# Optimization experiments

Measured on AMD Instinct MI355X. Metric: run time of the kernel, lower is better.

Reference implementation:

```python
import jax, jax.numpy as jnp
import numpy as np

B, LC, LQ, D = 32, 2048, 256, 256


def setup_inputs() -> dict:
    key = jax.random.key(0)
    kc, kq, kcm, kqm, kw = jax.random.split(key, 5)
    context = jax.random.normal(kc, (B, LC, D), dtype=jnp.float32)
    query = jax.random.normal(kq, (B, LQ, D), dtype=jnp.float32)
    # True = masked (matches torch masked_fill semantics)
    context_mask = jax.random.randint(kcm, (B, LC), 0, 2).astype(bool)
    query_mask = jax.random.randint(kqm, (B, LQ), 0, 2).astype(bool)
    # nn.Linear(3*dim, 1, bias=False) weight, flattened to (3D,)
    w0 = jax.random.normal(kw, (3 * D,), dtype=jnp.float32) * (1.0 / np.sqrt(3 * D))
    return {"context": context, "query": query, "context_mask": context_mask,
            "query_mask": query_mask, "w0": w0}


def reference(context, query, context_mask, query_mask, w0):
    d = context.shape[-1]
    wc, wq, wm = w0[:d], w0[d:2 * d], w0[2 * d:]
    # trilinear sim: w0 . [c, q, c*q]  ==  c.wc + q.wq + (c*wm) q^T
    sc = context @ wc                                   # (B, Lc)
    sq = query @ wq                                     # (B, Lq)
    sim = sc[:, :, None] + sq[:, None, :] + jnp.einsum(
        'bcd,bqd->bcq', context * wm, query)            # (B, Lc, Lq)
    mask = context_mask[:, :, None] | query_mask[:, None, :]
    sim = jnp.where(mask, jnp.float32(-1e30), sim)
    S = jax.nn.softmax(sim, axis=-1)                    # row softmax over Lq
    SS = jax.nn.softmax(sim, axis=1)                    # col softmax over Lc
    S = jnp.nan_to_num(S)
    SS = jnp.nan_to_num(SS)
    A = jnp.einsum('bcq,bqd->bcd', S, query)            # (B, Lc, D)
    T = jnp.einsum('bkq,bkd->bqd', SS, context)         # SS^T @ context, (B, Lq, D)
    Bmat = jnp.einsum('bcq,bqd->bcd', S, T)             # (B, Lc, D)
    return (A, Bmat)
```

## Files before the change

kernel.cpp:

```cpp
#include <hip/hip_runtime.h>

#define B_  32
#define LC_ 2048
#define LQ_ 256
#define D_  256
#define NEGH (-30000.0f)
#define MASKF (-100000.0f)

typedef _Float16 f16;
typedef _Float16 f16x4 __attribute__((ext_vector_type(4)));
typedef _Float16 f16x8 __attribute__((ext_vector_type(8)));
typedef float    f32x4 __attribute__((ext_vector_type(4)));

__global__ __launch_bounds__(256) void k_prepq(
    const float* __restrict__ qry, const float* __restrict__ w0,
    const int* __restrict__ qmask,
    f16* __restrict__ qrywm16, float* __restrict__ sqm,
    f16* __restrict__ Bcat)
{
    __shared__ float tile[32 * 260];
    __shared__ float wm_s[256], wq_s[256];
    const int b = blockIdx.y, q0 = blockIdx.x * 32;
    const int t = threadIdx.x;
    wm_s[t] = w0[2 * D_ + t];
    wq_s[t] = w0[D_ + t];
    __syncthreads();
    const int r = t >> 3, s = t & 7;
    const float* qb = qry + ((long long)(b * LQ_ + q0 + r)) * D_ + s * 32;
    f16* ob = qrywm16 + ((long long)(b * LQ_ + q0 + r)) * D_ + s * 32;
    float dot = 0.f;
    #pragma unroll
    for (int p = 0; p < 8; ++p) {
        float4 v = *(const float4*)(qb + p * 4);
        int cb = s * 32 + p * 4;
        f16x4 h;
        h[0] = (f16)(v.x * wm_s[cb + 0]); h[1] = (f16)(v.y * wm_s[cb + 1]);
        h[2] = (f16)(v.z * wm_s[cb + 2]); h[3] = (f16)(v.w * wm_s[cb + 3]);
        *(f16x4*)(ob + p * 4) = h;
        tile[r * 260 + cb + 0] = v.x;
        tile[r * 260 + cb + 1] = v.y;
        tile[r * 260 + cb + 2] = v.z;
        tile[r * 260 + cb + 3] = v.w;
        dot += v.x * wq_s[cb + 0] + v.y * wq_s[cb + 1]
             + v.z * wq_s[cb + 2] + v.w * wq_s[cb + 3];
    }
    dot += __shfl_xor(dot, 1, 64);
    dot += __shfl_xor(dot, 2, 64);
    dot += __shfl_xor(dot, 4, 64);
    if (s == 0) {
        int q = b * LQ_ + q0 + r;
        sqm[q] = qmask[q] ? MASKF : dot;
    }
    __syncthreads();
    {
        f16* orow = Bcat + (long long)b * 512 * LQ_ + (long long)t * LQ_ + q0;
        #pragma unroll
        for (int qq = 0; qq < 32; qq += 4) {
            f16x4 h;
            h[0] = (f16)tile[(qq + 0) * 260 + t];
            h[1] = (f16)tile[(qq + 1) * 260 + t];
            h[2] = (f16)tile[(qq + 2) * 260 + t];
            h[3] = (f16)tile[(qq + 3) * 260 + t];
            *(f16x4*)(orow + qq) = h;
        }
    }
}

#define LDA1 40
__global__ __launch_bounds__(512) void k_g1(
    const float* __restrict__ ctx, const f16* __restrict__ qrywm16,
    const float* __restrict__ w0, const int* __restrict__ cmask,
    const float* __restrict__ sqm,
    f16* __restrict__ ctxT16, f16* __restrict__ p16, f16* __restrict__ pT16,
    float* __restrict__ rowm, float* __restrict__ rowinvl,
    float* __restrict__ pm, float* __restrict__ pl)
{
    __shared__ f16 As[128 * LDA1];
    __shared__ f16 Bs[256 * LDA1];
    __shared__ float wc_s[256];
    __shared__ float scm_s[128];
    __shared__ float rowpm[4][128], rowps[4][128];
    __shared__ float colpm[2][256], colps[2][256];
    __shared__ float rowmax_s[128], colmax_s[256];
    const int b = blockIdx.z;
    const int c0 = blockIdx.x * 128;
    const int t = threadIdx.x, lane = t & 63, wv = t >> 6;
    const int wm_off = (wv >> 2) * 64, wn_off = (wv & 3) * 64;
    const float* Ab = ctx + ((long long)b * LC_ + c0) * D_;
    const f16* Bb = qrywm16 + (long long)b * LQ_ * D_;
    const int srow = t >> 2, scg = (t & 3) * 8;
    const int td = t & 31, tcc = t >> 5;
    if (t < 256) wc_s[t] = w0[t];
    __syncthreads();
    f32x4 acc[4][4] = {};
    float scdot = 0.f;
    for (int k0 = 0; k0 < D_; k0 += 32) {
        float4 a0 = *(const float4*)(Ab + (long long)srow * D_ + k0 + scg);
        float4 a1 = *(const float4*)(Ab + (long long)srow * D_ + k0 + scg + 4);
        f16x8 ha;
        ha[0] = (f16)a0.x; ha[1] = (f16)a0.y; ha[2] = (f16)a0.z; ha[3] = (f16)a0.w;
        ha[4] = (f16)a1.x; ha[5] = (f16)a1.y; ha[6] = (f16)a1.z; ha[7] = (f16)a1.w;
        scdot += a0.x * wc_s[k0 + scg + 0] + a0.y * wc_s[k0 + scg + 1]
               + a0.z * wc_s[k0 + scg + 2] + a0.w * wc_s[k0 + scg + 3]
               + a1.x * wc_s[k0 + scg + 4] + a1.y * wc_s[k0 + scg + 5]
               + a1.z * wc_s[k0 + scg + 6] + a1.w * wc_s[k0 + scg + 7];
        *(f16x8*)(As + srow * LDA1 + scg) = ha;
        *(f16x8*)(Bs + srow * LDA1 + scg) = *(const f16x8*)(Bb + (long long)srow * D_ + k0 + scg);
        *(f16x8*)(Bs + (srow + 128) * LDA1 + scg) = *(const f16x8*)(Bb + (long long)(srow + 128) * D_ + k0 + scg);
        __syncthreads();
        f16x8 af[4], bf[4];
        #pragma unroll
        for (int i = 0; i < 4; ++i)
            af[i] = *(const f16x8*)(As + (wm_off + i * 16 + (lane & 15)) * LDA1 + (lane >> 4) * 8);
        #pragma unroll
        for (int j = 0; j < 4; ++j)
            bf[j] = *(const f16x8*)(Bs + (wn_off + j * 16 + (lane & 15)) * LDA1 + (lane >> 4) * 8);
        #pragma unroll
        for (int i = 0; i < 4; ++i)
            #pragma unroll
            for (int j = 0; j < 4; ++j)
                acc[i][j] = __builtin_amdgcn_mfma_f32_16x16x32_f16(af[i], bf[j], acc[i][j], 0, 0, 0);
        {
            f16x8 hT;
            #pragma unroll
            for (int j = 0; j < 8; ++j)
                hT[j] = As[(tcc * 8 + j) * LDA1 + td];
            *(f16x8*)(ctxT16 + ((long long)b * D_ + k0 + td) * LC_ + c0 + tcc * 8) = hT;
        }
        __syncthreads();
    }
    scdot += __shfl_xor(scdot, 1, 64);
    scdot += __shfl_xor(scdot, 2, 64);
    if ((t & 3) == 0)
        scm_s[srow] = cmask[b * LC_ + c0 + srow] ? MASKF : scdot;
    __syncthreads();
    float sqv[4];
    #pragma unroll
    for (int j = 0; j < 4; ++j)
        sqv[j] = sqm[b * LQ_ + wn_off + j * 16 + (lane & 15)];
    float scv[4][4];
    #pragma unroll
    for (int i = 0; i < 4; ++i)
        #pragma unroll
        for (int r = 0; r < 4; ++r)
            scv[i][r] = scm_s[wm_off + i * 16 + (lane >> 4) * 4 + r];
    float rmax[4][4], cmax[4];
    #pragma unroll
    for (int i = 0; i < 4; ++i)
        #pragma unroll
        for (int r = 0; r < 4; ++r) rmax[i][r] = -INFINITY;
    #pragma unroll
    for (int j = 0; j < 4; ++j) cmax[j] = -INFINITY;
    #pragma unroll
    for (int i = 0; i < 4; ++i) {
        #pragma unroll
        for (int r = 0; r < 4; ++r) {
            #pragma unroll
            for (int j = 0; j < 4; ++j) {
                float val = fmaxf(acc[i][j][r] + scv[i][r] + sqv[j], NEGH);
                float vr = (float)(f16)val;
                rmax[i][r] = fmaxf(rmax[i][r], vr);
                cmax[j]    = fmaxf(cmax[j], vr);
            }
        }
    }
    #pragma unroll
    for (int i = 0; i < 4; ++i)
        #pragma unroll
        for (int r = 0; r < 4; ++r) {
            rmax[i][r] = fmaxf(rmax[i][r], __shfl_xor(rmax[i][r], 1, 64));
            rmax[i][r] = fmaxf(rmax[i][r], __shfl_xor(rmax[i][r], 2, 64));
            rmax[i][r] = fmaxf(rmax[i][r], __shfl_xor(rmax[i][r], 4, 64));
            rmax[i][r] = fmaxf(rmax[i][r], __shfl_xor(rmax[i][r], 8, 64));
        }
    #pragma unroll
    for (int j = 0; j < 4; ++j) {
        cmax[j] = fmaxf(cmax[j], __shfl_xor(cmax[j], 16, 64));
        cmax[j] = fmaxf(cmax[j], __shfl_xor(cmax[j], 32, 64));
    }
    if ((lane & 15) == 0) {
        #pragma unroll
        for (int i = 0; i < 4; ++i)
            #pragma unroll
            for (int r = 0; r < 4; ++r)
                rowpm[wv & 3][wm_off + i * 16 + (lane >> 4) * 4 + r] = rmax[i][r];
    }
    if (lane < 16) {
        #pragma unroll
        for (int j = 0; j < 4; ++j) colpm[wv >> 2][wn_off + j * 16 + lane] = cmax[j];
    }
    __syncthreads();
    if (t < 128)
        rowmax_s[t] = fmaxf(fmaxf(rowpm[0][t], rowpm[1][t]), fmaxf(rowpm[2][t], rowpm[3][t]));
    if (t < 256)
        colmax_s[t] = fmaxf(colpm[0][t], colpm[1][t]);
    __syncthreads();
    float rmf[4][4], cmf[4];
    #pragma unroll
    for (int i = 0; i < 4; ++i)
        #pragma unroll
        for (int r = 0; r < 4; ++r)
            rmf[i][r] = rowmax_s[wm_off + i * 16 + (lane >> 4) * 4 + r];
    #pragma unroll
    for (int j = 0; j < 4; ++j) cmf[j] = colmax_s[wn_off + j * 16 + (lane & 15)];
    float rsum[4][4] = {}, csum[4] = {};
    #pragma unroll
    for (int i = 0; i < 4; ++i) {
        #pragma unroll
        for (int r = 0; r < 4; ++r) {
            int c = c0 + wm_off + i * 16 + (lane >> 4) * 4 + r;
            f16* prow = p16 + ((long long)b * LC_ + c) * LQ_ + wn_off + (lane & 15);
            #pragma unroll
            for (int j = 0; j < 4; ++j) {
                int q = wn_off + j * 16 + (lane & 15);
                float val = fmaxf(acc[i][j][r] + scv[i][r] + sqv[j], NEGH);
                float vr = (float)(f16)val;
                float er = __expf(vr - rmf[i][r]);
                f16 hp = (f16)er;
                prow[j * 16] = hp;
                pT16[((long long)b * LQ_ + q) * LC_ + c] = hp;
                rsum[i][r] += er;
                csum[j]    += __expf(vr - cmf[j]);
            }
        }
    }
    #pragma unroll
    for (int i = 0; i < 4; ++i)
        #pragma unroll
        for (int r = 0; r < 4; ++r) {
            rsum[i][r] += __shfl_xor(rsum[i][r], 1, 64);
            rsum[i][r] += __shfl_xor(rsum[i][r], 2, 64);
            rsum[i][r] += __shfl_xor(rsum[i][r], 4, 64);
            rsum[i][r] += __shfl_xor(rsum[i][r], 8, 64);
        }
    #pragma unroll
    for (int j = 0; j < 4; ++j) {
        csum[j] += __shfl_xor(csum[j], 16, 64);
        csum[j] += __shfl_xor(csum[j], 32, 64);
    }
    if ((lane & 15) == 0) {
        #pragma unroll
        for (int i = 0; i < 4; ++i)
            #pragma unroll
            for (int r = 0; r < 4; ++r)
                rowps[wv & 3][wm_off + i * 16 + (lane >> 4) * 4 + r] = rsum[i][r];
    }
    if (lane < 16) {
        #pragma unroll
        for (int j = 0; j < 4; ++j) colps[wv >> 2][wn_off + j * 16 + lane] = csum[j];
    }
    __syncthreads();
    if (t < 128) {
        float l = rowps[0][t] + rowps[1][t] + rowps[2][t] + rowps[3][t];
        rowm[b * LC_ + c0 + t]    = rowmax_s[t];
        rowinvl[b * LC_ + c0 + t] = 1.0f / l;
    }
    if (t < 256) {
        int idx = (b * 16 + blockIdx.x) * LQ_ + t;
        pm[idx] = colmax_s[t];
        pl[idx] = colps[0][t] + colps[1][t];
    }
}

__global__ __launch_bounds__(256) void k_colreduce(
    const float* __restrict__ pm, const float* __restrict__ pl,
    float* __restrict__ colm, float* __restrict__ colinvl)
{
    const int col = blockIdx.x * 256 + threadIdx.x;
    const int b = col >> 8, q = col & 255;
    float M = -INFINITY, L = 0.f;
    for (int ch = 0; ch < 16; ++ch) {
        int idx = (b * 16 + ch) * LQ_ + q;
        float m = pm[idx], l = pl[idx];
        float nM = fmaxf(M, m);
        L = L * __expf(M - nM) + l * __expf(m - nM);
        M = nM;
    }
    colm[col] = M; colinvl[col] = 1.0f / L;
}

#define LDA3 72
#define G3SPLIT 4
#define G3CHUNK (LC_ / G3SPLIT)
__global__ __launch_bounds__(512) void k_g3(
    const f16* __restrict__ ctxT16, const f16* __restrict__ pT16,
    const float* __restrict__ rowm, const float* __restrict__ colm,
    float* __restrict__ Tpart)
{
    __shared__ f16 As[128 * LDA3];
    __shared__ f16 Bs[128 * LDA3];
    __shared__ float rowm_s[G3CHUNK];
    __shared__ float colm_s[128];
    const int lin = blockIdx.x;
    const int swz = (lin & 7) * 64 + (lin >> 3);
    const int combo = swz & 3;
    const int split = (swz >> 2) & 3;
    const int b = swz >> 4;
    const int qt = combo & 1, dh = combo >> 1;
    const int q0 = qt * 128, d0 = dh * 128;
    const int cbeg = split * G3CHUNK;
    const int t = threadIdx.x, lane = t & 63, wv = t >> 6;
    const int wm_off = (wv >> 2) * 64, wn_off = (wv & 3) * 32;
    if (t < G3CHUNK) rowm_s[t] = rowm[b * LC_ + cbeg + t];
    if (t < 128) colm_s[t] = colm[b * LQ_ + q0 + t];
    __syncthreads();
    const f16* Ab = ctxT16 + ((long long)b * D_ + d0) * LC_;
    const f16* Pb = pT16 + ((long long)b * LQ_ + q0) * LC_;
    const int ar = t >> 3, acg = (t & 7) * 8;
    f32x4 acc[4][2] = {};
    f16x8 ha[2], hb[2];
    #pragma unroll
    for (int p = 0; p < 2; ++p) {
        ha[p] = *(const f16x8*)(Ab + (long long)(ar + p * 64) * LC_ + cbeg + acg);
        hb[p] = *(const f16x8*)(Pb + (long long)(ar + p * 64) * LC_ + cbeg + acg);
    }
    for (int c0 = cbeg; c0 < cbeg + G3CHUNK; c0 += 64) {
        #pragma unroll
        for (int p = 0; p < 2; ++p) {
            *(f16x8*)(As + (ar + p * 64) * LDA3 + acg) = ha[p];
            float cmq = colm_s[ar + p * 64];
            f16x8 e;
            if (cmq < -29000.f) {
                #pragma unroll
                for (int j = 0; j < 8; ++j) e[j] = (f16)1.0f;
            } else {
                #pragma unroll
                for (int j = 0; j < 8; ++j)
                    e[j] = (f16)((float)hb[p][j] * __expf(rowm_s[(c0 - cbeg) + acg + j] - cmq));
            }
            *(f16x8*)(Bs + (ar + p * 64) * LDA3 + acg) = e;
        }
        if (c0 + 64 < cbeg + G3CHUNK) {
            #pragma unroll
            for (int p = 0; p < 2; ++p) {
                ha[p] = *(const f16x8*)(Ab + (long long)(ar + p * 64) * LC_ + c0 + 64 + acg);
                hb[p] = *(const f16x8*)(Pb + (long long)(ar + p * 64) * LC_ + c0 + 64 + acg);
            }
        }
        __syncthreads();
        #pragma unroll
        for (int kk = 0; kk < 64; kk += 32) {
            f16x8 af[4], bf[2];
            #pragma unroll
            for (int i = 0; i < 4; ++i)
                af[i] = *(const f16x8*)(As + (wm_off + i * 16 + (lane & 15)) * LDA3 + kk + (lane >> 4) * 8);
            #pragma unroll
            for (int j = 0; j < 2; ++j)
                bf[j] = *(const f16x8*)(Bs + (wn_off + j * 16 + (lane & 15)) * LDA3 + kk + (lane >> 4) * 8);
            #pragma unroll
            for (int i = 0; i < 4; ++i)
                #pragma unroll
                for (int j = 0; j < 2; ++j)
                    acc[i][j] = __builtin_amdgcn_mfma_f32_16x16x32_f16(af[i], bf[j], acc[i][j], 0, 0, 0);
        }
        __syncthreads();
    }
    float* Tb = Tpart + ((long long)split * B_ + b) * (LQ_ * D_);
    #pragma unroll
    for (int i = 0; i < 4; ++i) {
        #pragma unroll
        for (int r = 0; r < 4; ++r) {
            int d = d0 + wm_off + i * 16 + (lane >> 4) * 4 + r;
            float* orow = Tb + (long long)d * LQ_ + q0 + wn_off + (lane & 15);
            #pragma unroll
            for (int j = 0; j < 2; ++j)
                orow[j * 16] = acc[i][j][r];
        }
    }
}

__global__ __launch_bounds__(256) void k_bnorm(
    const float* __restrict__ Tpart, const float* __restrict__ colinvl,
    f16* __restrict__ Bcat)
{
    const long long i4 = ((long long)blockIdx.x * 256 + threadIdx.x) * 4;
    const int q = (int)(i4 & 255);
    const int d = (int)((i4 >> 8) & 255);
    const int b = (int)(i4 >> 16);
    float4 s = *(const float4*)(Tpart + i4);
    #pragma unroll
    for (int p = 1; p < G3SPLIT; ++p) {
        float4 v = *(const float4*)(Tpart + (long long)p * (B_ * LQ_ * D_) + i4);
        s.x += v.x; s.y += v.y; s.z += v.z; s.w += v.w;
    }
    float4 ci = *(const float4*)(colinvl + b * LQ_ + q);
    f16x4 h;
    h[0] = (f16)(s.x * ci.x); h[1] = (f16)(s.y * ci.y);
    h[2] = (f16)(s.z * ci.z); h[3] = (f16)(s.w * ci.w);
    *(f16x4*)(Bcat + (long long)b * 512 * LQ_ + (long long)(256 + d) * LQ_ + q) = h;
}

#define LDA23 40
__global__ __launch_bounds__(512) void k_g23(
    const f16* __restrict__ p16, const float* __restrict__ rowinvl,
    const f16* __restrict__ Bcat,
    float* __restrict__ outA, float* __restrict__ outB)
{
    __shared__ f16 As[256 * LDA23];
    __shared__ f16 Bs[256 * LDA23];
    const int lin = blockIdx.x;
    const int swz = (lin & 7) * 64 + (lin >> 3);
    const int cx = swz & 7;
    const int ny = (swz >> 3) & 1;
    const int b  = swz >> 4;
    const int c0 = cx * 256, n0 = ny * 256;
    const int t = threadIdx.x, lane = t & 63, wv = t >> 6;
    const int wm_off = (wv >> 2) * 128;
    const int wn_off = (wv & 3) * 64;
    const f16* Ab = p16 + ((long long)b * LC_ + c0) * LQ_;
    const f16* Bb = Bcat + ((long long)b * 512 + n0) * LQ_;
    const int srow = t >> 2, scg = (t & 3) * 8;
    f32x4 acc[8][4] = {};
    f16x8 ha[2], hb[2];
    #pragma unroll
    for (int p = 0; p < 2; ++p) {
        int r = srow + p * 128;
        ha[p] = *(const f16x8*)(Ab + (long long)r * LQ_ + scg);
        hb[p] = *(const f16x8*)(Bb + (long long)r * LQ_ + scg);
    }
    for (int k0 = 0; k0 < LQ_; k0 += 32) {
        #pragma unroll
        for (int p = 0; p < 2; ++p) {
            int r = srow + p * 128;
            *(f16x8*)(As + r * LDA23 + scg) = ha[p];
            *(f16x8*)(Bs + r * LDA23 + scg) = hb[p];
        }
        if (k0 + 32 < LQ_) {
            #pragma unroll
            for (int p = 0; p < 2; ++p) {
                int r = srow + p * 128;
                ha[p] = *(const f16x8*)(Ab + (long long)r * LQ_ + k0 + 32 + scg);
                hb[p] = *(const f16x8*)(Bb + (long long)r * LQ_ + k0 + 32 + scg);
            }
        }
        __syncthreads();
        f16x8 bf[4];
        #pragma unroll
        for (int j = 0; j < 4; ++j)
            bf[j] = *(const f16x8*)(Bs + (wn_off + j * 16 + (lane & 15)) * LDA23 + (lane >> 4) * 8);
        #pragma unroll
        for (int i = 0; i < 8; ++i) {
            f16x8 af = *(const f16x8*)(As + (wm_off + i * 16 + (lane & 15)) * LDA23 + (lane >> 4) * 8);
            #pragma unroll
            for (int j = 0; j < 4; ++j)
                acc[i][j] = __builtin_amdgcn_mfma_f32_16x16x32_f16(af, bf[j], acc[i][j], 0, 0, 0);
        }
        __syncthreads();
    }
    float* outp = (n0 == 0) ? outA : outB;
    #pragma unroll
    for (int i = 0; i < 8; ++i) {
        #pragma unroll
        for (int r = 0; r < 4; ++r) {
            int c = c0 + wm_off + i * 16 + (lane >> 4) * 4 + r;
            float ri = rowinvl[b * LC_ + c];
            float* orow = outp + ((long long)b * LC_ + c) * D_ + wn_off + (lane & 15);
            #pragma unroll
            for (int j = 0; j < 4; ++j)
                orow[j * 16] = acc[i][j][r] * ri;
        }
    }
}

extern "C" void kernel_launch(void* const* d_in, const int* in_sizes, int n_in,
                              void* d_out, int out_size, void* d_ws, size_t ws_size,
                              hipStream_t stream) {
    const float* ctx   = (const float*)d_in[0];
    const float* qry   = (const float*)d_in[1];
    const int*   cmask = (const int*)d_in[2];
    const int*   qmask = (const int*)d_in[3];
    const float* w0    = (const float*)d_in[4];
    float* out = (float*)d_out;

    char* w = (char*)d_ws;
    float* sqm     = (float*)w;  w += (long long)8192 * 4;
    float* rowm    = (float*)w;  w += (long long)65536 * 4;
    float* rowinvl = (float*)w;  w += (long long)65536 * 4;
    float* colm    = (float*)w;  w += (long long)8192 * 4;
    float* colinvl = (float*)w;  w += (long long)8192 * 4;
    float* pm      = (float*)w;  w += (long long)524288 * 4;
    float* pl      = (float*)w;  w += (long long)524288 * 4;
    f16*   p16     = (f16*)w;    w += (long long)16777216 * 2;
    f16*   pT16    = (f16*)w;    w += (long long)16777216 * 2;
    f16*   ctxT16  = (f16*)w;    w += (long long)16777216 * 2;
    f16*   qrywm16 = (f16*)w;    w += (long long)2097152 * 2;
    f16*   Bcat    = (f16*)w;    w += (long long)4194304 * 2;
    float* Tpart   = (float*)w;  w += (long long)G3SPLIT * 2097152 * 4;

    k_prepq<<<dim3(8, 32), 256, 0, stream>>>(qry, w0, qmask, qrywm16, sqm, Bcat);
    k_g1<<<dim3(16, 1, 32), 512, 0, stream>>>(ctx, qrywm16, w0, cmask, sqm,
        ctxT16, p16, pT16, rowm, rowinvl, pm, pl);
    k_colreduce<<<32, 256, 0, stream>>>(pm, pl, colm, colinvl);
    k_g3<<<512, 512, 0, stream>>>(ctxT16, pT16, rowm, colm, Tpart);
    k_bnorm<<<2048, 256, 0, stream>>>(Tpart, colinvl, Bcat);
    k_g23<<<512, 512, 0, stream>>>(p16, rowinvl, Bcat,
        out, out + (long long)B_ * LC_ * D_);
}
```

Measured before the change: 300.1 us.

## Drop transposed P copy, read row-major P in g3, atomically reduce T splits

k_g1 no longer writes the transposed fp16 probability matrix pT16, which was a scattered 2-byte-stride store of 32 MB. k_g3 now reads row-major p16 and transposes it into shared memory while applying the column-softmax rescale. The four split-K partial T buffers are replaced by one buffer that is zeroed first and accumulated with float atomics, so k_bnorm reads a quarter of the data. Column reduction is also restructured into a two-pass max-then-sum. The costs are scalar 2-byte transposed LDS stores with likely bank conflicts, atomic contention, and a nondeterministic summation order.

Measured after the change: 305.9 us. About the same (+2.0%).

```diff
diff --git a/kernel.cpp b/kernel.cpp
--- a/kernel.cpp
+++ b/kernel.cpp
@@ -11,6 +11,13 @@
 typedef _Float16 f16x4 __attribute__((ext_vector_type(4)));
 typedef _Float16 f16x8 __attribute__((ext_vector_type(8)));
 typedef float    f32x4 __attribute__((ext_vector_type(4)));
+
+__global__ __launch_bounds__(256) void k_zero(float* __restrict__ T)
+{
+    const long long i4 = ((long long)blockIdx.x * 256 + threadIdx.x) * 4;
+    float4 z = {0.f, 0.f, 0.f, 0.f};
+    *(float4*)(T + i4) = z;
+}
 
 __global__ __launch_bounds__(256) void k_prepq(
     const float* __restrict__ qry, const float* __restrict__ w0,
@@ -71,7 +78,7 @@
     const float* __restrict__ ctx, const f16* __restrict__ qrywm16,
     const float* __restrict__ w0, const int* __restrict__ cmask,
     const float* __restrict__ sqm,
-    f16* __restrict__ ctxT16, f16* __restrict__ p16, f16* __restrict__ pT16,
+    f16* __restrict__ ctxT16, f16* __restrict__ p16,
     float* __restrict__ rowm, float* __restrict__ rowinvl,
     float* __restrict__ pm, float* __restrict__ pl)
 {
@@ -212,13 +219,10 @@
             f16* prow = p16 + ((long long)b * LC_ + c) * LQ_ + wn_off + (lane & 15);
             #pragma unroll
             for (int j = 0; j < 4; ++j) {
-                int q = wn_off + j * 16 + (lane & 15);
                 float val = fmaxf(acc[i][j][r] + scv[i][r] + sqv[j], NEGH);
                 float vr = (float)(f16)val;
                 float er = __expf(vr - rmf[i][r]);
-                f16 hp = (f16)er;
-                prow[j * 16] = hp;
-                pT16[((long long)b * LQ_ + q) * LC_ + c] = hp;
+                prow[j * 16] = (f16)er;
                 rsum[i][r] += er;
                 csum[j]    += __expf(vr - cmf[j]);
             }
@@ -268,14 +272,19 @@
 {
     const int col = blockIdx.x * 256 + threadIdx.x;
     const int b = col >> 8, q = col & 255;
-    float M = -INFINITY, L = 0.f;
+    float m[16], l[16];
+    #pragma unroll
     for (int ch = 0; ch < 16; ++ch) {
         int idx = (b * 16 + ch) * LQ_ + q;
-        float m = pm[idx], l = pl[idx];
-        float nM = fmaxf(M, m);
-        L = L * __expf(M - nM) + l * __expf(m - nM);
-        M = nM;
-    }
+        m[ch] = pm[idx];
+        l[ch] = pl[idx];
+    }
+    float M = m[0];
+    #pragma unroll
+    for (int ch = 1; ch < 16; ++ch) M = fmaxf(M, m[ch]);
+    float L = 0.f;
+    #pragma unroll
+    for (int ch = 0; ch < 16; ++ch) L += l[ch] * __expf(m[ch] - M);
     colm[col] = M; colinvl[col] = 1.0f / L;
 }
 
@@ -283,9 +292,9 @@
 #define G3SPLIT 4
 #define G3CHUNK (LC_ / G3SPLIT)
 __global__ __launch_bounds__(512) void k_g3(
-    const f16* __restrict__ ctxT16, const f16* __restrict__ pT16,
+    const f16* __restrict__ ctxT16, const f16* __restrict__ p16,
     const float* __restrict__ rowm, const float* __restrict__ colm,
-    float* __restrict__ Tpart)
+    float* __restrict__ T)
 {
     __shared__ f16 As[128 * LDA3];
     __shared__ f16 Bs[128 * LDA3];
@@ -305,37 +314,37 @@
     if (t < 128) colm_s[t] = colm[b * LQ_ + q0 + t];
     __syncthreads();
     const f16* Ab = ctxT16 + ((long long)b * D_ + d0) * LC_;
-    const f16* Pb = pT16 + ((long long)b * LQ_ + q0) * LC_;
+    const f16* Pb = p16 + (long long)b * LC_ * LQ_;
     const int ar = t >> 3, acg = (t & 7) * 8;
+    const int cr = lane, qg = wv;
     f32x4 acc[4][2] = {};
-    f16x8 ha[2], hb[2];
-    #pragma unroll
-    for (int p = 0; p < 2; ++p) {
-        ha[p] = *(const f16x8*)(Ab + (long long)(ar + p * 64) * LC_ + cbeg + acg);
-        hb[p] = *(const f16x8*)(Pb + (long long)(ar + p * 64) * LC_ + cbeg + acg);
-    }
+    f16x8 ha[2], hbq[2];
+    ha[0] = *(const f16x8*)(Ab + (long long)(ar +  0) * LC_ + cbeg + acg);
+    ha[1] = *(const f16x8*)(Ab + (long long)(ar + 64) * LC_ + cbeg + acg);
+    hbq[0] = *(const f16x8*)(Pb + (long long)(cbeg + cr) * LQ_ + q0 + qg * 16);
+    hbq[1] = *(const f16x8*)(Pb + (long long)(cbeg + cr) * LQ_ + q0 + qg * 16 + 8);
     for (int c0 = cbeg; c0 < cbeg + G3CHUNK; c0 += 64) {
-        #pragma unroll
-        for (int p = 0; p < 2; ++p) {
-            *(f16x8*)(As + (ar + p * 64) * LDA3 + acg) = ha[p];
-            float cmq = colm_s[ar + p * 64];
-            f16x8 e;
-            if (cmq < -29000.f) {
+        *(f16x8*)(As + (ar +  0) * LDA3 + acg) = ha[0];
+        *(f16x8*)(As + (ar + 64) * LDA3 + acg) = ha[1];
+        {
+            float rmv = rowm_s[(c0 - cbeg) + cr];
+            #pragma unroll
+            for (int u = 0; u < 2; ++u) {
                 #pragma unroll
-                for (int j = 0; j < 8; ++j) e[j] = (f16)1.0f;
-            } else {
-                #pragma unroll
-                for (int j = 0; j < 8; ++j)
-                    e[j] = (f16)((float)hb[p][j] * __expf(rowm_s[(c0 - cbeg) + acg + j] - cmq));
+                for (int k = 0; k < 8; ++k) {
+                    int qq = qg * 16 + u * 8 + k;
+                    float cmq = colm_s[qq];
+                    float v = (cmq < -29000.f) ? 1.0f
+                            : (float)hbq[u][k] * __expf(rmv - cmq);
+                    Bs[qq * LDA3 + cr] = (f16)v;
+                }
             }
-            *(f16x8*)(Bs + (ar + p * 64) * LDA3 + acg) = e;
         }
         if (c0 + 64 < cbeg + G3CHUNK) {
-            #pragma unroll
-            for (int p = 0; p < 2; ++p) {
-                ha[p] = *(const f16x8*)(Ab + (long long)(ar + p * 64) * LC_ + c0 + 64 + acg);
-                hb[p] = *(const f16x8*)(Pb + (long long)(ar + p * 64) * LC_ + c0 + 64 + acg);
-            }
+            ha[0] = *(const f16x8*)(Ab + (long long)(ar +  0) * LC_ + c0 + 64 + acg);
+            ha[1] = *(const f16x8*)(Ab + (long long)(ar + 64) * LC_ + c0 + 64 + acg);
+            hbq[0] = *(const f16x8*)(Pb + (long long)(c0 + 64 + cr) * LQ_ + q0 + qg * 16);
+            hbq[1] = *(const f16x8*)(Pb + (long long)(c0 + 64 + cr) * LQ_ + q0 + qg * 16 + 8);
         }
         __syncthreads();
         #pragma unroll
@@ -355,7 +364,7 @@
         }
         __syncthreads();
     }
-    float* Tb = Tpart + ((long long)split * B_ + b) * (LQ_ * D_);
+    float* Tb = T + (long long)b * (D_ * LQ_);
     #pragma unroll
     for (int i = 0; i < 4; ++i) {
         #pragma unroll
@@ -364,25 +373,20 @@
             float* orow = Tb + (long long)d * LQ_ + q0 + wn_off + (lane & 15);
             #pragma unroll
             for (int j = 0; j < 2; ++j)
-                orow[j * 16] = acc[i][j][r];
+                unsafeAtomicAdd(orow + j * 16, acc[i][j][r]);
         }
     }
 }
 
 __global__ __launch_bounds__(256) void k_bnorm(
-    const float* __restrict__ Tpart, const float* __restrict__ colinvl,
+    const float* __restrict__ T, const float* __restrict__ colinvl,
     f16* __restrict__ Bcat)
 {
     const long long i4 = ((long long)blockIdx.x * 256 + threadIdx.x) * 4;
     const int q = (int)(i4 & 255);
     const int d = (int)((i4 >> 8) & 255);
     const int b = (int)(i4 >> 16);
-    float4 s = *(const float4*)(Tpart + i4);
-    #pragma unroll
-    for (int p = 1; p < G3SPLIT; ++p) {
-        float4 v = *(const float4*)(Tpart + (long long)p * (B_ * LQ_ * D_) + i4);
-        s.x += v.x; s.y += v.y; s.z += v.z; s.w += v.w;
-    }
+    float4 s = *(const float4*)(T + i4);
     float4 ci = *(const float4*)(colinvl + b * LQ_ + q);
     f16x4 h;
     h[0] = (f16)(s.x * ci.x); h[1] = (f16)(s.y * ci.y);
@@ -481,18 +485,18 @@
     float* pm      = (float*)w;  w += (long long)524288 * 4;
     float* pl      = (float*)w;  w += (long long)524288 * 4;
     f16*   p16     = (f16*)w;    w += (long long)16777216 * 2;
-    f16*   pT16    = (f16*)w;    w += (long long)16777216 * 2;
     f16*   ctxT16  = (f16*)w;    w += (long long)16777216 * 2;
     f16*   qrywm16 = (f16*)w;    w += (long long)2097152 * 2;
     f16*   Bcat    = (f16*)w;    w += (long long)4194304 * 2;
-    float* Tpart   = (float*)w;  w += (long long)G3SPLIT * 2097152 * 4;
-
+    float* T       = (float*)w;  w += (long long)2097152 * 4;
+
+    k_zero<<<2048, 256, 0, stream>>>(T);
     k_prepq<<<dim3(8, 32), 256, 0, stream>>>(qry, w0, qmask, qrywm16, sqm, Bcat);
     k_g1<<<dim3(16, 1, 32), 512, 0, stream>>>(ctx, qrywm16, w0, cmask, sqm,
-        ctxT16, p16, pT16, rowm, rowinvl, pm, pl);
+        ctxT16, p16, rowm, rowinvl, pm, pl);
     k_colreduce<<<32, 256, 0, stream>>>(pm, pl, colm, colinvl);
-    k_g3<<<512, 512, 0, stream>>>(ctxT16, pT16, rowm, colm, Tpart);
-    k_bnorm<<<2048, 256, 0, stream>>>(Tpart, colinvl, Bcat);
+    k_g3<<<512, 512, 0, stream>>>(ctxT16, p16, rowm, colm, T);
+    k_bnorm<<<2048, 256, 0, stream>>>(T, colinvl, Bcat);
     k_g23<<<512, 512, 0, stream>>>(p16, rowinvl, Bcat,
         out, out + (long long)B_ * LC_ * D_);
 }
```
